# Performance work log

Hardware: AMD Instinct MI355X
Metric: run time of the kernel (lower is better)

The kernel has to match this reference:

```python
import jax, jax.numpy as jnp
import numpy as np

D = 1024
B, L = 4, 2048
H = 4  # num_heads
EPS = 1e-5


def setup_inputs() -> dict:
    key = jax.random.key(0)
    ks = jax.random.split(key, 32)
    s = 0.02
    def w(k, shp):
        return jax.random.normal(k, shp, dtype=jnp.float32) * s
    inp = {
        "features": jax.random.normal(ks[0], (B, L, D), dtype=jnp.float32),
        "action_mask": jax.random.randint(ks[1], (B, L), 0, 2, dtype=jnp.int32),
        "dial_mask": jax.random.randint(ks[2], (B, L), 0, 2, dtype=jnp.int32),
        "ent_mask": jax.random.randint(ks[3], (B, L), 0, 2, dtype=jnp.int32),
        "head_mask": jax.random.randint(ks[4], (B, L), 0, 2, dtype=jnp.int32),
        # 4 modality projections (stored as [in, out])
        "Wa": w(ks[5], (D, D)), "ba": jnp.zeros((D,), jnp.float32),
        "Wd": w(ks[6], (D, D)), "bd": jnp.zeros((D,), jnp.float32),
        "We": w(ks[7], (D, D)), "be": jnp.zeros((D,), jnp.float32),
        "Wh": w(ks[8], (D, D)), "bh": jnp.zeros((D,), jnp.float32),
        # MultiheadAttention in/out projections
        "Wq": w(ks[9], (D, D)), "bq": jnp.zeros((D,), jnp.float32),
        "Wk": w(ks[10], (D, D)), "bk": jnp.zeros((D,), jnp.float32),
        "Wv": w(ks[11], (D, D)), "bv": jnp.zeros((D,), jnp.float32),
        "Wo": w(ks[12], (D, D)), "bo": jnp.zeros((D,), jnp.float32),
        # consensus gate MLP: 4D -> 2D -> D
        "Wg1": w(ks[13], (4 * D, 2 * D)), "bg1": jnp.zeros((2 * D,), jnp.float32),
        "Wg2": w(ks[14], (2 * D, D)), "bg2": jnp.zeros((D,), jnp.float32),
        # LayerNorm
        "ln_g": jnp.ones((D,), jnp.float32), "ln_b": jnp.zeros((D,), jnp.float32),
    }
    return inp


def _forward(features, action_mask, dial_mask, ent_mask, head_mask,
             Wa, ba, Wd, bd, We, be, Wh, bh,
             Wq, bq, Wk, bk, Wv, bv, Wo, bo,
             Wg1, bg1, Wg2, bg2, ln_g, ln_b):
    b, l, d = features.shape
    hd = d // H
    masks = [action_mask, dial_mask, ent_mask, head_mask]
    proj = [(Wa, ba), (Wd, bd), (We, be), (Wh, bh)]
    # masked linear projections -> [B,L,4,D]
    mods = [
        (features @ W + bias) * m[..., None].astype(features.dtype)
        for (W, bias), m in zip(proj, masks)
    ]
    x = jnp.stack(mods, axis=2).reshape(b * l, 4, d)  # [N,4,D], N=B*L
    # tiny self-attention over the 4 modality tokens (dropout inactive / eval)
    q = (x @ Wq + bq).reshape(-1, 4, H, hd)
    k = (x @ Wk + bk).reshape(-1, 4, H, hd)
    v = (x @ Wv + bv).reshape(-1, 4, H, hd)
    scores = jnp.einsum('nqhd,nkhd->nhqk', q, k) / jnp.sqrt(jnp.float32(hd)).astype(x.dtype)
    attn = jax.nn.softmax(scores, axis=-1)
    ctx = jnp.einsum('nhqk,nkhd->nqhd', attn, v).reshape(-1, 4, d)
    attended = (ctx @ Wo + bo).reshape(b, l, 4 * d)
    # gate MLP (exact erf GELU, matching nn.GELU default)
    h = jax.nn.gelu(attended @ Wg1 + bg1, approximate=False)
    consensus = h @ Wg2 + bg2
    # residual + LayerNorm
    y = features + consensus
    mu = jnp.mean(y, axis=-1, keepdims=True)
    var = jnp.mean(jnp.square(y - mu), axis=-1, keepdims=True)
    return (y - mu) / jnp.sqrt(var + EPS) * ln_g + ln_b


def reference(features, action_mask, dial_mask, ent_mask, head_mask,
              Wa, ba, Wd, bd, We, be, Wh, bh,
              Wq, bq, Wk, bk, Wv, bv, Wo, bo,
              Wg1, bg1, Wg2, bg2, ln_g, ln_b):
    return _forward(features, action_mask, dial_mask, ent_mask, head_mask,
                    Wa, ba, Wd, bd, We, be, Wh, bh,
                    Wq, bq, Wk, bk, Wv, bv, Wo, bo,
                    Wg1, bg1, Wg2, bg2, ln_g, ln_b)
```

## Files before the change

### kernel.cpp

```cpp
#include <hip/hip_runtime.h>
#include <cstdint>
#include <cstddef>

#define DM   1024
#define NT   8192
#define HD   256
#define BM 128
#define BN 128
#define BK 64

typedef __attribute__((ext_vector_type(4))) float f32x4;
typedef __attribute__((ext_vector_type(8))) short bf16x8;

#define MF(a_, b_, c_) __builtin_amdgcn_mfma_f32_16x16x32_bf16(a_, b_, c_, 0, 0, 0)

__device__ __forceinline__ unsigned short f2bf(float f) {
    union { float f; uint32_t u; } v; v.f = f;
    return (unsigned short)((v.u + 0x7fffu + ((v.u >> 16) & 1u)) >> 16);
}
__device__ __forceinline__ float bf2f(unsigned short h) {
    union { uint32_t u; float f; } v; v.u = ((uint32_t)h) << 16;
    return v.f;
}

template <int SWZ>
__device__ __forceinline__ int2 swz_xy() {
    int wid = blockIdx.y * gridDim.x + blockIdx.x;
    const int nwg = gridDim.x * gridDim.y;
    int2 r;
    if (SWZ == 1 && (gridDim.x & 7) == 0) {
        const int sx = gridDim.x >> 3;
        const int c = wid & 7;
        const int l = wid >> 3;
        r.x = c * sx + l % sx;
        r.y = l / sx;
        return r;
    }
    if ((nwg & 7) == 0) {
        const int per = nwg >> 3;
        wid = (wid & 7) * per + (wid >> 3);
    }
    r.x = wid % gridDim.x;
    r.y = wid / gridDim.x;
    return r;
}

struct Ptr4 { const float* p[4]; };
struct Mask4 { const int* p[4]; };

__global__ void cvt_f32_to_bf16(const float* __restrict__ src,
                                unsigned short* __restrict__ dst, int n4) {
    int i = blockIdx.x * blockDim.x + threadIdx.x;
    if (i >= n4) return;
    float4 v = reinterpret_cast<const float4*>(src)[i];
    ushort4 o;
    o.x = f2bf(v.x); o.y = f2bf(v.y); o.z = f2bf(v.z); o.w = f2bf(v.w);
    reinterpret_cast<ushort4*>(dst)[i] = o;
}

__global__ void cvt5_f32_to_bf16(Ptr4 w4, const float* __restrict__ wo,
                                 unsigned short* __restrict__ wcat,
                                 unsigned short* __restrict__ wobf) {
    const int i = blockIdx.x * blockDim.x + threadIdx.x;
    const int w = i >> 18, r = i & 262143;
    const float* src = (w < 4) ? w4.p[w] : wo;
    unsigned short* dst = (w < 4) ? (wcat + ((size_t)w << 20)) : wobf;
    float4 v = reinterpret_cast<const float4*>(src)[r];
    ushort4 o;
    o.x = f2bf(v.x); o.y = f2bf(v.y); o.z = f2bf(v.z); o.w = f2bf(v.w);
    reinterpret_cast<ushort4*>(dst)[r] = o;
}

__global__ void transpose_cvt(const float* __restrict__ src,
                              unsigned short* __restrict__ dst, int K, int Nc) {
    __shared__ float tile[32][33];
    const int n0 = blockIdx.x * 32, k0 = blockIdx.y * 32;
    const int tx = threadIdx.x & 31, ty = threadIdx.x >> 5;
#pragma unroll
    for (int i = 0; i < 4; ++i) {
        int k = ty + i * 8;
        tile[k][tx] = src[(size_t)(k0 + k) * Nc + n0 + tx];
    }
    __syncthreads();
#pragma unroll
    for (int i = 0; i < 4; ++i) {
        int n = ty + i * 8;
        dst[(size_t)(n0 + n) * K + k0 + tx] = f2bf(tile[tx][n]);
    }
}

__device__ __forceinline__ void gload16(const void* g, void* l) {
    __builtin_amdgcn_global_load_lds(
        (const __attribute__((address_space(1))) void*)g,
        (__attribute__((address_space(3))) void*)l, 16, 0, 0);
}

template <int EPI, int SWZ = 0>
__global__ void gemm_bt(const unsigned short* __restrict__ A,
                        const unsigned short* __restrict__ Bt,
                        void* __restrict__ out, Ptr4 bias, Mask4 masks,
                        const float* __restrict__ biasA,
                        int M, int Nc, int K) {
    __shared__ __attribute__((aligned(16))) unsigned short Als[BM * BK];
    __shared__ __attribute__((aligned(16))) unsigned short Bls[BN * BK];
    const int tid = threadIdx.x;
    const int wave = tid >> 6, lane = tid & 63;
    const int2 bxy = swz_xy<SWZ>();
    const int tileM = bxy.y * BM, tileN = bxy.x * BN;
    const int wr = wave >> 1, wc = wave & 1;
    const int la = lane & 15, lh = lane >> 4;

    f32x4 acc[4][4] = {};

    const int sr = tid >> 3;
    const int sb = (tid & 7) * 16;
    const int ssw = (sb ^ ((sr & 7) << 4)) >> 1;
    const unsigned short* aSrcs[4];
    const unsigned short* bSrcs[4];
#pragma unroll
    for (int c = 0; c < 4; ++c) {
        aSrcs[c] = A + (size_t)(tileM + c * 32 + sr) * K + ssw;
        bSrcs[c] = Bt + (size_t)(tileN + c * 32 + sr) * K + ssw;
    }

    for (int k0 = 0; k0 < K; k0 += BK) {
#pragma unroll
        for (int c = 0; c < 4; ++c)
            gload16(aSrcs[c] + k0, &Als[wave * 512 + c * 2048]);
#pragma unroll
        for (int c = 0; c < 4; ++c)
            gload16(bSrcs[c] + k0, &Bls[wave * 512 + c * 2048]);
        __syncthreads();
#pragma unroll
        for (int ks = 0; ks < 2; ++ks) {
            const int uo = ((ks * 4 + lh) ^ (la & 7)) * 8;
            bf16x8 af[4], bfr[4];
#pragma unroll
            for (int m = 0; m < 4; ++m)
                af[m] = *reinterpret_cast<const bf16x8*>(&Als[(wr * 64 + m * 16 + la) * BK + uo]);
#pragma unroll
            for (int n = 0; n < 4; ++n)
                bfr[n] = *reinterpret_cast<const bf16x8*>(&Bls[(wc * 64 + n * 16 + la) * BK + uo]);
#pragma unroll
            for (int m = 0; m < 4; ++m)
#pragma unroll
                for (int n = 0; n < 4; ++n)
                    acc[m][n] = MF(af[m], bfr[n], acc[m][n]);
        }
        __syncthreads();
    }

    const int rowT = tileM + wr * 64 + lh * 4;
    const int colT = tileN + wc * 64;
    unsigned short* outB = (unsigned short*)out;
    float* outF = (float*)out;

    float mv[4][4];
    if constexpr (EPI == 0 || EPI == 5) {
        const int* mp = (EPI == 0) ? masks.p[tileN >> 10] : masks.p[(tileN >> 10) & 3];
#pragma unroll
        for (int m = 0; m < 4; ++m)
#pragma unroll
            for (int i = 0; i < 4; ++i)
                mv[m][i] = (float)mp[rowT + m * 16 + i];
    }
    const float* bp = nullptr;
    const float* bp2 = nullptr;
    if constexpr (EPI == 5) bp2 = bias.p[tileN >> 12];
    else bp = bias.p[tileN >> 10];

#pragma unroll
    for (int n = 0; n < 4; ++n) {
        const int gcol = colT + n * 16 + la;
        float bv, bv2 = 0.f;
        if constexpr (EPI == 5) { bv = biasA[gcol]; bv2 = bp2[gcol & (DM - 1)]; }
        else bv = bp[gcol & (DM - 1)];
#pragma unroll
        for (int m = 0; m < 4; ++m) {
#pragma unroll
            for (int i = 0; i < 4; ++i) {
                const int grow = rowT + m * 16 + i;
                float val = acc[m][n][i] + bv;
                if constexpr (EPI == 0) {
                    val *= mv[m][i];
                    outB[(size_t)grow * Nc + gcol] = f2bf(val);
                } else if constexpr (EPI == 1) {
                    outB[(size_t)grow * Nc + gcol] = f2bf(val);
                } else if constexpr (EPI == 2) {
                    val = 0.5f * val * (1.0f + erff(val * 0.70710678118654752f));
                    outB[(size_t)grow * Nc + gcol] = f2bf(val);
                } else if constexpr (EPI == 3) {
                    outF[(size_t)grow * Nc + gcol] = val;
                } else {
                    val = mv[m][i] * val + bv2;
                    outB[(size_t)grow * Nc + gcol] = f2bf(val);
                }
            }
        }
    }
}

template <bool TSTORE>
__global__ void gemm_prep(const unsigned short* __restrict__ A0, int lda, int aZoff,
                          const unsigned short* __restrict__ Bt, int ldb,
                          unsigned short* __restrict__ out, int ldc, int cZstride,
                          int K) {
    __shared__ __attribute__((aligned(16))) unsigned short Als[BM * BK];
    __shared__ __attribute__((aligned(16))) unsigned short Bls[BN * BK];
    const unsigned short* A = A0 + (size_t)blockIdx.z * aZoff;
    const int tid = threadIdx.x;
    const int wave = tid >> 6, lane = tid & 63;
    const int2 bxy = swz_xy<0>();
    const int tileM = bxy.y * BM, tileN = bxy.x * BN;
    const int wr = wave >> 1, wc = wave & 1;
    const int la = lane & 15, lh = lane >> 4;

    f32x4 acc[4][4] = {};

    const int sr = tid >> 3;
    const int sb = (tid & 7) * 16;
    const int ssw = (sb ^ ((sr & 7) << 4)) >> 1;
    const unsigned short* aSrcs[4];
    const unsigned short* bSrcs[4];
#pragma unroll
    for (int c = 0; c < 4; ++c) {
        aSrcs[c] = A + (size_t)(tileM + c * 32 + sr) * lda + ssw;
        bSrcs[c] = Bt + (size_t)(tileN + c * 32 + sr) * ldb + ssw;
    }

    for (int k0 = 0; k0 < K; k0 += BK) {
#pragma unroll
        for (int c = 0; c < 4; ++c)
            gload16(aSrcs[c] + k0, &Als[wave * 512 + c * 2048]);
#pragma unroll
        for (int c = 0; c < 4; ++c)
            gload16(bSrcs[c] + k0, &Bls[wave * 512 + c * 2048]);
        __syncthreads();
#pragma unroll
        for (int ks = 0; ks < 2; ++ks) {
            const int uo = ((ks * 4 + lh) ^ (la & 7)) * 8;
            bf16x8 af[4], bfr[4];
#pragma unroll
            for (int m = 0; m < 4; ++m)
                af[m] = *reinterpret_cast<const bf16x8*>(&Als[(wr * 64 + m * 16 + la) * BK + uo]);
#pragma unroll
            for (int n = 0; n < 4; ++n)
                bfr[n] = *reinterpret_cast<const bf16x8*>(&Bls[(wc * 64 + n * 16 + la) * BK + uo]);
#pragma unroll
            for (int m = 0; m < 4; ++m)
#pragma unroll
                for (int n = 0; n < 4; ++n)
                    acc[m][n] = MF(af[m], bfr[n], acc[m][n]);
        }
        __syncthreads();
    }

    const int rowT = tileM + wr * 64 + lh * 4;
    const int colT = tileN + wc * 64;

#pragma unroll
    for (int n = 0; n < 4; ++n) {
        const int gcol = colT + n * 16 + la;
#pragma unroll
        for (int m = 0; m < 4; ++m) {
            if constexpr (TSTORE) {
                const int g0 = rowT + m * 16;
                ushort4 o4;
                o4.x = f2bf(acc[m][n][0]);
                o4.y = f2bf(acc[m][n][1]);
                o4.z = f2bf(acc[m][n][2]);
                o4.w = f2bf(acc[m][n][3]);
                const size_t drow = ((size_t)(gcol >> 10) << 12) +
                                    ((size_t)(g0 >> 10) << 10) + (gcol & 1023);
                *reinterpret_cast<ushort4*>(out + drow * 1024 + (g0 & 1023)) = o4;
            } else {
#pragma unroll
                for (int i = 0; i < 4; ++i) {
                    const int grow = rowT + m * 16 + i;
                    out[(size_t)grow * ldc + (size_t)blockIdx.z * cZstride + gcol] =
                        f2bf(acc[m][n][i]);
                }
            }
        }
    }
}

__global__ void fuse_biasA(Ptr4 bmods, const unsigned short* __restrict__ Btqkv,
                           float* __restrict__ biasA) {
    const int o = blockIdx.x * 4 + (threadIdx.x >> 6);
    const int lane = threadIdx.x & 63;
    const int qk = o >> 12, im = (o >> 10) & 3, j = o & 1023;
    const float* b = bmods.p[im];
    const unsigned short* wrow = Btqkv + ((size_t)(qk << 10) + j) * 1024;
    float s = 0.f;
    for (int t = lane; t < 1024; t += 64) s += b[t] * bf2f(wrow[t]);
#pragma unroll
    for (int off = 32; off >= 1; off >>= 1) s += __shfl_xor(s, off, 64);
    if (lane == 0) biasA[o] = s;
}

__global__ void fuse_biasH(const float* __restrict__ bo, const float* __restrict__ bg1,
                           const unsigned short* __restrict__ Btg1,
                           float* __restrict__ biasH) {
    const int c = blockIdx.x * 4 + (threadIdx.x >> 6);
    const int lane = threadIdx.x & 63;
    const unsigned short* row = Btg1 + (size_t)c * 4096;
    float s = 0.f;
    for (int t = lane; t < 4096; t += 64) s += bo[t & 1023] * bf2f(row[t]);
#pragma unroll
    for (int off = 32; off >= 1; off >>= 1) s += __shfl_xor(s, off, 64);
    if (lane == 0) biasH[c] = s + bg1[c];
}

__global__ void attn4F(const unsigned short* __restrict__ qkvF,
                       unsigned short* __restrict__ ctx) {
    const int n = blockIdx.x;
    const int h = threadIdx.x >> 6;
    const int lane = threadIdx.x & 63;
    const size_t base = (size_t)n * 12288 + h * HD + lane * 4;

    float q[4][4], k[4][4], v[4][4];
#pragma unroll
    for (int m = 0; m < 4; ++m) {
        ushort4 uq = *reinterpret_cast<const ushort4*>(&qkvF[base + m * 1024]);
        ushort4 uk = *reinterpret_cast<const ushort4*>(&qkvF[base + m * 1024 + 4096]);
        ushort4 uv = *reinterpret_cast<const ushort4*>(&qkvF[base + m * 1024 + 8192]);
        q[m][0] = bf2f(uq.x); q[m][1] = bf2f(uq.y); q[m][2] = bf2f(uq.z); q[m][3] = bf2f(uq.w);
        k[m][0] = bf2f(uk.x); k[m][1] = bf2f(uk.y); k[m][2] = bf2f(uk.z); k[m][3] = bf2f(uk.w);
        v[m][0] = bf2f(uv.x); v[m][1] = bf2f(uv.y); v[m][2] = bf2f(uv.z); v[m][3] = bf2f(uv.w);
    }

    float s[4][4];
#pragma unroll
    for (int qi = 0; qi < 4; ++qi)
#pragma unroll
        for (int ki = 0; ki < 4; ++ki)
            s[qi][ki] = q[qi][0] * k[ki][0] + q[qi][1] * k[ki][1] +
                        q[qi][2] * k[ki][2] + q[qi][3] * k[ki][3];
#pragma unroll
    for (int off = 32; off >= 1; off >>= 1) {
#pragma unroll
        for (int qi = 0; qi < 4; ++qi)
#pragma unroll
            for (int ki = 0; ki < 4; ++ki)
                s[qi][ki] += __shfl_xor(s[qi][ki], off, 64);
    }

#pragma unroll
    for (int qi = 0; qi < 4; ++qi) {
        float s0 = s[qi][0] * 0.0625f, s1 = s[qi][1] * 0.0625f;
        float s2 = s[qi][2] * 0.0625f, s3 = s[qi][3] * 0.0625f;
        float mx = fmaxf(fmaxf(s0, s1), fmaxf(s2, s3));
        float e0 = __expf(s0 - mx), e1 = __expf(s1 - mx);
        float e2 = __expf(s2 - mx), e3 = __expf(s3 - mx);
        float inv = 1.0f / (e0 + e1 + e2 + e3);
        e0 *= inv; e1 *= inv; e2 *= inv; e3 *= inv;
        ushort4 o;
        o.x = f2bf(e0 * v[0][0] + e1 * v[1][0] + e2 * v[2][0] + e3 * v[3][0]);
        o.y = f2bf(e0 * v[0][1] + e1 * v[1][1] + e2 * v[2][1] + e3 * v[3][1]);
        o.z = f2bf(e0 * v[0][2] + e1 * v[1][2] + e2 * v[2][2] + e3 * v[3][2]);
        o.w = f2bf(e0 * v[0][3] + e1 * v[1][3] + e2 * v[2][3] + e3 * v[3][3]);
        *reinterpret_cast<ushort4*>(&ctx[(size_t)n * 4096 + qi * 1024 + h * HD + lane * 4]) = o;
    }
}

__global__ void attn4(const unsigned short* __restrict__ qkv,
                      unsigned short* __restrict__ ctx) {
    const int n = blockIdx.x;
    const int h = threadIdx.x >> 6;
    const int lane = threadIdx.x & 63;
    const size_t base = (size_t)n * 4 * 3072 + h * HD + lane * 4;

    float q[4][4], k[4][4], v[4][4];
#pragma unroll
    for (int m = 0; m < 4; ++m) {
        ushort4 uq = *reinterpret_cast<const ushort4*>(&qkv[base + (size_t)m * 3072]);
        ushort4 uk = *reinterpret_cast<const ushort4*>(&qkv[base + (size_t)m * 3072 + 1024]);
        ushort4 uv = *reinterpret_cast<const ushort4*>(&qkv[base + (size_t)m * 3072 + 2048]);
        q[m][0] = bf2f(uq.x); q[m][1] = bf2f(uq.y); q[m][2] = bf2f(uq.z); q[m][3] = bf2f(uq.w);
        k[m][0] = bf2f(uk.x); k[m][1] = bf2f(uk.y); k[m][2] = bf2f(uk.z); k[m][3] = bf2f(uk.w);
        v[m][0] = bf2f(uv.x); v[m][1] = bf2f(uv.y); v[m][2] = bf2f(uv.z); v[m][3] = bf2f(uv.w);
    }

    float s[4][4];
#pragma unroll
    for (int qi = 0; qi < 4; ++qi)
#pragma unroll
        for (int ki = 0; ki < 4; ++ki)
            s[qi][ki] = q[qi][0] * k[ki][0] + q[qi][1] * k[ki][1] +
                        q[qi][2] * k[ki][2] + q[qi][3] * k[ki][3];
#pragma unroll
    for (int off = 32; off >= 1; off >>= 1) {
#pragma unroll
        for (int qi = 0; qi < 4; ++qi)
#pragma unroll
            for (int ki = 0; ki < 4; ++ki)
                s[qi][ki] += __shfl_xor(s[qi][ki], off, 64);
    }

#pragma unroll
    for (int qi = 0; qi < 4; ++qi) {
        float s0 = s[qi][0] * 0.0625f, s1 = s[qi][1] * 0.0625f;
        float s2 = s[qi][2] * 0.0625f, s3 = s[qi][3] * 0.0625f;
        float mx = fmaxf(fmaxf(s0, s1), fmaxf(s2, s3));
        float e0 = __expf(s0 - mx), e1 = __expf(s1 - mx);
        float e2 = __expf(s2 - mx), e3 = __expf(s3 - mx);
        float inv = 1.0f / (e0 + e1 + e2 + e3);
        e0 *= inv; e1 *= inv; e2 *= inv; e3 *= inv;
        ushort4 o;
        o.x = f2bf(e0 * v[0][0] + e1 * v[1][0] + e2 * v[2][0] + e3 * v[3][0]);
        o.y = f2bf(e0 * v[0][1] + e1 * v[1][1] + e2 * v[2][1] + e3 * v[3][1]);
        o.z = f2bf(e0 * v[0][2] + e1 * v[1][2] + e2 * v[2][2] + e3 * v[3][2]);
        o.w = f2bf(e0 * v[0][3] + e1 * v[1][3] + e2 * v[2][3] + e3 * v[3][3]);
        *reinterpret_cast<ushort4*>(&ctx[(size_t)(n * 4 + qi) * 1024 + h * HD + lane * 4]) = o;
    }
}

__global__ void resid_ln(const float* __restrict__ cons, const float* __restrict__ feat,
                         const float* __restrict__ g, const float* __restrict__ b,
                         float* __restrict__ out) {
    const int row = blockIdx.x;
    const int t = threadIdx.x;
    const size_t base = (size_t)row * DM + t * 4;
    float4 c = *reinterpret_cast<const float4*>(&cons[base]);
    float4 f = *reinterpret_cast<const float4*>(&feat[base]);
    float y0 = c.x + f.x, y1 = c.y + f.y, y2 = c.z + f.z, y3 = c.w + f.w;
    float sum = y0 + y1 + y2 + y3;
    float sq = y0 * y0 + y1 * y1 + y2 * y2 + y3 * y3;
#pragma unroll
    for (int off = 32; off >= 1; off >>= 1) {
        sum += __shfl_xor(sum, off, 64);
        sq += __shfl_xor(sq, off, 64);
    }
    __shared__ float rs[4], rq[4];
    const int wv = t >> 6, ln = t & 63;
    if (ln == 0) { rs[wv] = sum; rq[wv] = sq; }
    __syncthreads();
    sum = rs[0] + rs[1] + rs[2] + rs[3];
    sq = rq[0] + rq[1] + rq[2] + rq[3];
    const float mu = sum * (1.0f / DM);
    const float var = sq * (1.0f / DM) - mu * mu;
    const float rstd = rsqrtf(var + 1e-5f);
    float4 gg = *reinterpret_cast<const float4*>(&g[t * 4]);
    float4 bb = *reinterpret_cast<const float4*>(&b[t * 4]);
    float4 o;
    o.x = (y0 - mu) * rstd * gg.x + bb.x;
    o.y = (y1 - mu) * rstd * gg.y + bb.y;
    o.z = (y2 - mu) * rstd * gg.z + bb.z;
    o.w = (y3 - mu) * rstd * gg.w + bb.w;
    *reinterpret_cast<float4*>(&out[base]) = o;
}

extern "C" void kernel_launch(void* const* d_in, const int* in_sizes, int n_in,
                              void* d_out, int out_size, void* d_ws, size_t ws_size,
                              hipStream_t stream) {
    (void)in_sizes; (void)n_in; (void)out_size;
    const float* feat = (const float*)d_in[0];
    const int* am = (const int*)d_in[1];
    const int* dmk = (const int*)d_in[2];
    const int* em = (const int*)d_in[3];
    const int* hmk = (const int*)d_in[4];
    const float* Wa = (const float*)d_in[5];  const float* ba = (const float*)d_in[6];
    const float* Wd = (const float*)d_in[7];  const float* bd = (const float*)d_in[8];
    const float* We = (const float*)d_in[9];  const float* be = (const float*)d_in[10];
    const float* Wh = (const float*)d_in[11]; const float* bh = (const float*)d_in[12];
    const float* Wq = (const float*)d_in[13]; const float* bq = (const float*)d_in[14];
    const float* Wk = (const float*)d_in[15]; const float* bk = (const float*)d_in[16];
    const float* Wv = (const float*)d_in[17]; const float* bv = (const float*)d_in[18];
    const float* Wo = (const float*)d_in[19]; const float* bo = (const float*)d_in[20];
    const float* Wg1 = (const float*)d_in[21]; const float* bg1 = (const float*)d_in[22];
    const float* Wg2 = (const float*)d_in[23]; const float* bg2 = (const float*)d_in[24];
    const float* lng = (const float*)d_in[25]; const float* lnb = (const float*)d_in[26];

    char* ws = (char*)d_ws;
    size_t off = 0;
    auto take = [&](size_t bytes) -> char* {
        char* r = ws + off;
        off = (off + bytes + 255) & ~(size_t)255;
        return r;
    };
    unsigned short* featB = (unsigned short*)take((size_t)NT * DM * 2);
    unsigned short* Btqkv = (unsigned short*)take((size_t)3 * DM * DM * 2);
    unsigned short* Btg1  = (unsigned short*)take((size_t)2 * DM * 4 * DM * 2);
    unsigned short* Btg2  = (unsigned short*)take((size_t)DM * 2 * DM * 2);
    unsigned short* Wcat  = (unsigned short*)take((size_t)4 * DM * DM * 2);
    unsigned short* Wo_bf = (unsigned short*)take((size_t)DM * DM * 2);
    unsigned short* Btf   = (unsigned short*)take((size_t)12 * DM * DM * 2);
    unsigned short* Btm1  = (unsigned short*)take((size_t)8 * DM * DM * 2);
    float* biasA          = (float*)take((size_t)12 * DM * 4);
    float* biasH          = (float*)take((size_t)2 * DM * 4);
    const size_t fixed = off;

    cvt_f32_to_bf16<<<dim3((NT * DM / 4 + 255) / 256), dim3(256), 0, stream>>>(
        feat, featB, NT * DM / 4);
    auto tl = [&](const float* src, unsigned short* dst, int K, int Nc) {
        transpose_cvt<<<dim3(Nc / 32, K / 32), dim3(256), 0, stream>>>(src, dst, K, Nc);
    };
    tl(Wq, Btqkv, DM, DM);
    tl(Wk, Btqkv + (size_t)DM * DM, DM, DM);
    tl(Wv, Btqkv + (size_t)2 * DM * DM, DM, DM);
    tl(Wg1, Btg1, 4 * DM, 2 * DM);
    tl(Wg2, Btg2, 2 * DM, DM);

    Ptr4 bmods{{ba, bd, be, bh}};
    Ptr4 bqkv{{bq, bk, bv, nullptr}};
    Ptr4 bH{{biasH, biasH + DM, nullptr, nullptr}};
    Ptr4 bg24{{bg2, nullptr, nullptr, nullptr}};
    Mask4 mnull{{nullptr, nullptr, nullptr, nullptr}};

    const size_t ctxBytes = (size_t)NT * 4096 * 2;
    const size_t hBytes = (size_t)NT * 2048 * 2 + 512;
    int T2 = 0;
    {
        const int cands[4] = {8192, 4096, 2048, 1024};
        for (int ci = 0; ci < 4; ++ci) {
            int c = cands[ci];
            size_t chunkB = (size_t)c * 24576 + 512;
            size_t regHB = chunkB > hBytes ? chunkB : hBytes;
            if (fixed + ctxBytes + 256 + regHB + 4096 <= ws_size) { T2 = c; break; }
        }
    }

    if (T2 > 0) {
        char* regX = take(ctxBytes);
        size_t chunkB = (size_t)T2 * 24576 + 512;
        char* regH = take(chunkB > hBytes ? chunkB : hBytes);
        unsigned short* ctx = (unsigned short*)regX;
        float* cons = (float*)regX;
        unsigned short* h = (unsigned short*)regH;
        unsigned short* qkvF = (unsigned short*)regH;

        Ptr4 w4{{Wa, Wd, We, Wh}};
        cvt5_f32_to_bf16<<<dim3(5 * DM * DM / 4 / 256), dim3(256), 0, stream>>>(
            w4, Wo, Wcat, Wo_bf);
        gemm_prep<true><<<dim3(24, 32, 1), dim3(256), 0, stream>>>(
            Wcat, DM, 0, Btqkv, DM, Btf, 0, 0, DM);
        gemm_prep<false><<<dim3(8, 16, 4), dim3(256), 0, stream>>>(
            Btg1, 4 * DM, DM, Wo_bf, DM, Btm1, 4 * DM, DM, DM);
        fuse_biasA<<<dim3(12 * DM / 4), dim3(256), 0, stream>>>(bmods, Btqkv, biasA);
        fuse_biasH<<<dim3(2 * DM / 4), dim3(256), 0, stream>>>(bo, bg1, Btg1, biasH);

        for (int t0 = 0; t0 < NT; t0 += T2) {
            Mask4 mk{{am + t0, dmk + t0, em + t0, hmk + t0}};
            gemm_bt<5, 1><<<dim3(96, T2 / BM), dim3(256), 0, stream>>>(
                featB + (size_t)t0 * DM, Btf, (void*)qkvF, bqkv, mk, biasA,
                T2, 12 * DM, DM);
            attn4F<<<dim3(T2), dim3(256), 0, stream>>>(qkvF, ctx + (size_t)t0 * 4096);
        }
        gemm_bt<2><<<dim3(16, NT / BM), dim3(256), 0, stream>>>(
            ctx, Btm1, (void*)h, bH, mnull, nullptr, NT, 2 * DM, 4 * DM);
        gemm_bt<3><<<dim3(8, NT / BM), dim3(256), 0, stream>>>(
            h, Btg2, (void*)cons, bg24, mnull, nullptr, NT, DM, 2 * DM);
        resid_ln<<<dim3(NT), dim3(256), 0, stream>>>(cons, feat, lng, lnb, (float*)d_out);
        return;
    }

    unsigned short* Bt1 = (unsigned short*)take((size_t)4 * DM * DM * 2);
    unsigned short* Bto = (unsigned short*)take((size_t)DM * DM * 2);
    tl(Wa, Bt1, DM, DM);
    tl(Wd, Bt1 + (size_t)DM * DM, DM, DM);
    tl(We, Bt1 + (size_t)2 * DM * DM, DM, DM);
    tl(Wh, Bt1 + (size_t)3 * DM * DM, DM, DM);
    tl(Wo, Bto, DM, DM);

    Ptr4 b1{{ba, bd, be, bh}};
    Ptr4 bo4{{bo, nullptr, nullptr, nullptr}};
    Ptr4 bg14{{bg1, bg1 + DM, nullptr, nullptr}};

    const size_t avail = (ws_size > off) ? (ws_size - off) : 0;
    int T = 2048;
    while (T > 128 && ((size_t)T * 40960 + 4096) > avail) T >>= 1;
    unsigned short* bufA = (unsigned short*)take((size_t)T * 4096 * 2);
    unsigned short* bufB = (unsigned short*)take((size_t)T * 4 * 3072 * 2);
    unsigned short* bufC = (unsigned short*)take((size_t)T * 4 * 1024 * 2);

    const int nch = NT / T;
    for (int c = 0; c < nch; ++c) {
        const int t0 = c * T;
        Mask4 mk{{am + t0, dmk + t0, em + t0, hmk + t0}};
        gemm_bt<0><<<dim3(4 * DM / BN, T / BM), dim3(256), 0, stream>>>(
            featB + (size_t)t0 * DM, Bt1, (void*)bufA, b1, mk, nullptr, T, 4 * DM, DM);
        gemm_bt<1><<<dim3(3 * DM / BN, 4 * T / BM), dim3(256), 0, stream>>>(
            bufA, Btqkv, (void*)bufB, bqkv, mnull, nullptr, 4 * T, 3 * DM, DM);
        attn4<<<dim3(T), dim3(256), 0, stream>>>(bufB, bufC);
        gemm_bt<1><<<dim3(DM / BN, 4 * T / BM), dim3(256), 0, stream>>>(
            bufC, Bto, (void*)bufA, bo4, mnull, nullptr, 4 * T, DM, DM);
        gemm_bt<2><<<dim3(2 * DM / BN, T / BM), dim3(256), 0, stream>>>(
            bufA, Btg1, (void*)bufC, bg14, mnull, nullptr, T, 2 * DM, 4 * DM);
        gemm_bt<3><<<dim3(DM / BN, T / BM), dim3(256), 0, stream>>>(
            bufC, Btg2, (void*)bufB, bg24, mnull, nullptr, T, DM, 2 * DM);
        resid_ln<<<dim3(T), dim3(256), 0, stream>>>(
            (const float*)bufB, feat + (size_t)t0 * DM, lng, lnb,
            (float*)d_out + (size_t)t0 * DM);
    }
}
```

Baseline: 588.5 us.

## Switch GEMMs to 32x32x16 MFMA with fragment-major LDS layout; bf16 consensus output

Both GEMM kernels move from 16x16x32 MFMA with a 4x4 accumulator grid to 32x32x16 MFMA with a 2x2 grid of 16-wide accumulators. Global-to-LDS loads are rearranged so each 32-row by 8-column fragment is stored contiguously, letting each lane read its operand with one linear LDS access and no XOR swizzle. The aim is fewer MFMA and LDS instructions per K step. Separately, the consensus GEMM now writes bf16 instead of fp32 and the residual LayerNorm reads bf16, halving that buffer's traffic at the cost of some precision before the normalization.

Measured after the change: 988.1 us. +67.9%, slower.

```diff
diff --git a/kernel.cpp b/kernel.cpp
--- a/kernel.cpp
+++ b/kernel.cpp
@@ -10,9 +10,10 @@
 #define BK 64
 
 typedef __attribute__((ext_vector_type(4))) float f32x4;
+typedef __attribute__((ext_vector_type(16))) float f32x16;
 typedef __attribute__((ext_vector_type(8))) short bf16x8;
 
-#define MF(a_, b_, c_) __builtin_amdgcn_mfma_f32_16x16x32_bf16(a_, b_, c_, 0, 0, 0)
+#define MF32(a_, b_, c_) __builtin_amdgcn_mfma_f32_32x32x16_bf16(a_, b_, c_, 0, 0, 0)
 
 __device__ __forceinline__ unsigned short f2bf(float f) {
     union { float f; uint32_t u; } v; v.f = f;
@@ -108,92 +109,84 @@
     const int2 bxy = swz_xy<SWZ>();
     const int tileM = bxy.y * BM, tileN = bxy.x * BN;
     const int wr = wave >> 1, wc = wave & 1;
-    const int la = lane & 15, lh = lane >> 4;
-
-    f32x4 acc[4][4] = {};
-
-    const int sr = tid >> 3;
-    const int sb = (tid & 7) * 16;
-    const int ssw = (sb ^ ((sr & 7) << 4)) >> 1;
+    const int la32 = lane & 31, lh32 = lane >> 5;
+
+    f32x16 acc[2][2] = {};
+
     const unsigned short* aSrcs[4];
     const unsigned short* bSrcs[4];
 #pragma unroll
-    for (int c = 0; c < 4; ++c) {
-        aSrcs[c] = A + (size_t)(tileM + c * 32 + sr) * K + ssw;
-        bSrcs[c] = Bt + (size_t)(tileN + c * 32 + sr) * K + ssw;
+    for (int r = 0; r < 4; ++r) {
+        aSrcs[r] = A + (size_t)(tileM + r * 32 + la32) * K + wave * 16 + lh32 * 8;
+        bSrcs[r] = Bt + (size_t)(tileN + r * 32 + la32) * K + wave * 16 + lh32 * 8;
     }
 
     for (int k0 = 0; k0 < K; k0 += BK) {
 #pragma unroll
-        for (int c = 0; c < 4; ++c)
-            gload16(aSrcs[c] + k0, &Als[wave * 512 + c * 2048]);
-#pragma unroll
-        for (int c = 0; c < 4; ++c)
-            gload16(bSrcs[c] + k0, &Bls[wave * 512 + c * 2048]);
+        for (int r = 0; r < 4; ++r)
+            gload16(aSrcs[r] + k0, &Als[r * 2048 + wave * 512]);
+#pragma unroll
+        for (int r = 0; r < 4; ++r)
+            gload16(bSrcs[r] + k0, &Bls[r * 2048 + wave * 512]);
         __syncthreads();
 #pragma unroll
-        for (int ks = 0; ks < 2; ++ks) {
-            const int uo = ((ks * 4 + lh) ^ (la & 7)) * 8;
-            bf16x8 af[4], bfr[4];
-#pragma unroll
-            for (int m = 0; m < 4; ++m)
-                af[m] = *reinterpret_cast<const bf16x8*>(&Als[(wr * 64 + m * 16 + la) * BK + uo]);
-#pragma unroll
-            for (int n = 0; n < 4; ++n)
-                bfr[n] = *reinterpret_cast<const bf16x8*>(&Bls[(wc * 64 + n * 16 + la) * BK + uo]);
-#pragma unroll
-            for (int m = 0; m < 4; ++m)
-#pragma unroll
-                for (int n = 0; n < 4; ++n)
-                    acc[m][n] = MF(af[m], bfr[n], acc[m][n]);
+        for (int ks = 0; ks < 4; ++ks) {
+            bf16x8 af[2], bfr[2];
+#pragma unroll
+            for (int mt = 0; mt < 2; ++mt)
+                af[mt] = *reinterpret_cast<const bf16x8*>(
+                    &Als[((wr * 2 + mt) * 4 + ks) * 512 + lane * 8]);
+#pragma unroll
+            for (int nt = 0; nt < 2; ++nt)
+                bfr[nt] = *reinterpret_cast<const bf16x8*>(
+                    &Bls[((wc * 2 + nt) * 4 + ks) * 512 + lane * 8]);
+#pragma unroll
+            for (int mt = 0; mt < 2; ++mt)
+#pragma unroll
+                for (int nt = 0; nt < 2; ++nt)
+                    acc[mt][nt] = MF32(af[mt], bfr[nt], acc[mt][nt]);
         }
         __syncthreads();
     }
 
-    const int rowT = tileM + wr * 64 + lh * 4;
-    const int colT = tileN + wc * 64;
     unsigned short* outB = (unsigned short*)out;
-    float* outF = (float*)out;
-
-    float mv[4][4];
-    if constexpr (EPI == 0 || EPI == 5) {
-        const int* mp = (EPI == 0) ? masks.p[tileN >> 10] : masks.p[(tileN >> 10) & 3];
-#pragma unroll
-        for (int m = 0; m < 4; ++m)
-#pragma unroll
-            for (int i = 0; i < 4; ++i)
-                mv[m][i] = (float)mp[rowT + m * 16 + i];
-    }
+    const int* mp = nullptr;
+    if constexpr (EPI == 0) mp = masks.p[tileN >> 10];
+    if constexpr (EPI == 5) mp = masks.p[(tileN >> 10) & 3];
     const float* bp = nullptr;
     const float* bp2 = nullptr;
     if constexpr (EPI == 5) bp2 = bias.p[tileN >> 12];
     else bp = bias.p[tileN >> 10];
 
 #pragma unroll
-    for (int n = 0; n < 4; ++n) {
-        const int gcol = colT + n * 16 + la;
+    for (int nt = 0; nt < 2; ++nt) {
+        const int gcol = tileN + (wc * 2 + nt) * 32 + la32;
         float bv, bv2 = 0.f;
         if constexpr (EPI == 5) { bv = biasA[gcol]; bv2 = bp2[gcol & (DM - 1)]; }
         else bv = bp[gcol & (DM - 1)];
 #pragma unroll
-        for (int m = 0; m < 4; ++m) {
-#pragma unroll
-            for (int i = 0; i < 4; ++i) {
-                const int grow = rowT + m * 16 + i;
-                float val = acc[m][n][i] + bv;
-                if constexpr (EPI == 0) {
-                    val *= mv[m][i];
-                    outB[(size_t)grow * Nc + gcol] = f2bf(val);
-                } else if constexpr (EPI == 1) {
-                    outB[(size_t)grow * Nc + gcol] = f2bf(val);
-                } else if constexpr (EPI == 2) {
-                    val = 0.5f * val * (1.0f + erff(val * 0.70710678118654752f));
-                    outB[(size_t)grow * Nc + gcol] = f2bf(val);
-                } else if constexpr (EPI == 3) {
-                    outF[(size_t)grow * Nc + gcol] = val;
-                } else {
-                    val = mv[m][i] * val + bv2;
-                    outB[(size_t)grow * Nc + gcol] = f2bf(val);
+        for (int mt = 0; mt < 2; ++mt) {
+#pragma unroll
+            for (int rg = 0; rg < 4; ++rg) {
+                const int rowb = tileM + (wr * 2 + mt) * 32 + lh32 * 4 + rg * 8;
+#pragma unroll
+                for (int i = 0; i < 4; ++i) {
+                    const int grow = rowb + i;
+                    float val = acc[mt][nt][rg * 4 + i] + bv;
+                    if constexpr (EPI == 0) {
+                        val *= (float)mp[grow];
+                        outB[(size_t)grow * Nc + gcol] = f2bf(val);
+                    } else if constexpr (EPI == 1) {
+                        outB[(size_t)grow * Nc + gcol] = f2bf(val);
+                    } else if constexpr (EPI == 2) {
+                        val = 0.5f * val * (1.0f + erff(val * 0.70710678118654752f));
+                        outB[(size_t)grow * Nc + gcol] = f2bf(val);
+                    } else if constexpr (EPI == 3) {
+                        outB[(size_t)grow * Nc + gcol] = f2bf(val);
+                    } else {
+                        val = (float)mp[grow] * val + bv2;
+                        outB[(size_t)grow * Nc + gcol] = f2bf(val);
+                    }
                 }
             }
         }
@@ -213,72 +206,70 @@
     const int2 bxy = swz_xy<0>();
     const int tileM = bxy.y * BM, tileN = bxy.x * BN;
     const int wr = wave >> 1, wc = wave & 1;
-    const int la = lane & 15, lh = lane >> 4;
-
-    f32x4 acc[4][4] = {};
-
-    const int sr = tid >> 3;
-    const int sb = (tid & 7) * 16;
-    const int ssw = (sb ^ ((sr & 7) << 4)) >> 1;
+    const int la32 = lane & 31, lh32 = lane >> 5;
+
+    f32x16 acc[2][2] = {};
+
     const unsigned short* aSrcs[4];
     const unsigned short* bSrcs[4];
 #pragma unroll
-    for (int c = 0; c < 4; ++c) {
-        aSrcs[c] = A + (size_t)(tileM + c * 32 + sr) * lda + ssw;
-        bSrcs[c] = Bt + (size_t)(tileN + c * 32 + sr) * ldb + ssw;
+    for (int r = 0; r < 4; ++r) {
+        aSrcs[r] = A + (size_t)(tileM + r * 32 + la32) * lda + wave * 16 + lh32 * 8;
+        bSrcs[r] = Bt + (size_t)(tileN + r * 32 + la32) * ldb + wave * 16 + lh32 * 8;
     }
 
     for (int k0 = 0; k0 < K; k0 += BK) {
 #pragma unroll
-        for (int c = 0; c < 4; ++c)
-            gload16(aSrcs[c] + k0, &Als[wave * 512 + c * 2048]);
-#pragma unroll
-        for (int c = 0; c < 4; ++c)
-            gload16(bSrcs[c] + k0, &Bls[wave * 512 + c * 2048]);
+        for (int r = 0; r < 4; ++r)
+            gload16(aSrcs[r] + k0, &Als[r * 2048 + wave * 512]);
+#pragma unroll
+        for (int r = 0; r < 4; ++r)
+            gload16(bSrcs[r] + k0, &Bls[r * 2048 + wave * 512]);
         __syncthreads();
 #pragma unroll
-        for (int ks = 0; ks < 2; ++ks) {
-            const int uo = ((ks * 4 + lh) ^ (la & 7)) * 8;
-            bf16x8 af[4], bfr[4];
-#pragma unroll
-            for (int m = 0; m < 4; ++m)
-                af[m] = *reinterpret_cast<const bf16x8*>(&Als[(wr * 64 + m * 16 + la) * BK + uo]);
-#pragma unroll
-            for (int n = 0; n < 4; ++n)
-                bfr[n] = *reinterpret_cast<const bf16x8*>(&Bls[(wc * 64 + n * 16 + la) * BK + uo]);
-#pragma unroll
-            for (int m = 0; m < 4; ++m)
-#pragma unroll
-                for (int n = 0; n < 4; ++n)
-                    acc[m][n] = MF(af[m], bfr[n], acc[m][n]);
+        for (int ks = 0; ks < 4; ++ks) {
+            bf16x8 af[2], bfr[2];
+#pragma unroll
+            for (int mt = 0; mt < 2; ++mt)
+                af[mt] = *reinterpret_cast<const bf16x8*>(
+                    &Als[((wr * 2 + mt) * 4 + ks) * 512 + lane * 8]);
+#pragma unroll
+            for (int nt = 0; nt < 2; ++nt)
+                bfr[nt] = *reinterpret_cast<const bf16x8*>(
+                    &Bls[((wc * 2 + nt) * 4 + ks) * 512 + lane * 8]);
+#pragma unroll
+            for (int mt = 0; mt < 2; ++mt)
+#pragma unroll
+                for (int nt = 0; nt < 2; ++nt)
+                    acc[mt][nt] = MF32(af[mt], bfr[nt], acc[mt][nt]);
         }
         __syncthreads();
     }
 
-    const int rowT = tileM + wr * 64 + lh * 4;
-    const int colT = tileN + wc * 64;
-
-#pragma unroll
-    for (int n = 0; n < 4; ++n) {
-        const int gcol = colT + n * 16 + la;
-#pragma unroll
-        for (int m = 0; m < 4; ++m) {
-            if constexpr (TSTORE) {
-                const int g0 = rowT + m * 16;
-                ushort4 o4;
-                o4.x = f2bf(acc[m][n][0]);
-                o4.y = f2bf(acc[m][n][1]);
-                o4.z = f2bf(acc[m][n][2]);
-                o4.w = f2bf(acc[m][n][3]);
-                const size_t drow = ((size_t)(gcol >> 10) << 12) +
-                                    ((size_t)(g0 >> 10) << 10) + (gcol & 1023);
-                *reinterpret_cast<ushort4*>(out + drow * 1024 + (g0 & 1023)) = o4;
-            } else {
-#pragma unroll
-                for (int i = 0; i < 4; ++i) {
-                    const int grow = rowT + m * 16 + i;
-                    out[(size_t)grow * ldc + (size_t)blockIdx.z * cZstride + gcol] =
-                        f2bf(acc[m][n][i]);
+#pragma unroll
+    for (int nt = 0; nt < 2; ++nt) {
+        const int gcol = tileN + (wc * 2 + nt) * 32 + la32;
+#pragma unroll
+        for (int mt = 0; mt < 2; ++mt) {
+#pragma unroll
+            for (int rg = 0; rg < 4; ++rg) {
+                const int g0 = tileM + (wr * 2 + mt) * 32 + lh32 * 4 + rg * 8;
+                if constexpr (TSTORE) {
+                    ushort4 o4;
+                    o4.x = f2bf(acc[mt][nt][rg * 4 + 0]);
+                    o4.y = f2bf(acc[mt][nt][rg * 4 + 1]);
+                    o4.z = f2bf(acc[mt][nt][rg * 4 + 2]);
+                    o4.w = f2bf(acc[mt][nt][rg * 4 + 3]);
+                    const size_t drow = ((size_t)(gcol >> 10) << 12) +
+                                        ((size_t)(g0 >> 10) << 10) + (gcol & 1023);
+                    *reinterpret_cast<ushort4*>(out + drow * 1024 + (g0 & 1023)) = o4;
+                } else {
+#pragma unroll
+                    for (int i = 0; i < 4; ++i) {
+                        const int grow = g0 + i;
+                        out[(size_t)grow * ldc + (size_t)blockIdx.z * cZstride + gcol] =
+                            f2bf(acc[mt][nt][rg * 4 + i]);
+                    }
                 }
             }
         }
@@ -416,15 +407,17 @@
     }
 }
 
-__global__ void resid_ln(const float* __restrict__ cons, const float* __restrict__ feat,
+__global__ void resid_ln(const unsigned short* __restrict__ cons,
+                         const float* __restrict__ feat,
                          const float* __restrict__ g, const float* __restrict__ b,
                          float* __restrict__ out) {
     const int row = blockIdx.x;
     const int t = threadIdx.x;
     const size_t base = (size_t)row * DM + t * 4;
-    float4 c = *reinterpret_cast<const float4*>(&cons[base]);
+    ushort4 c4 = *reinterpret_cast<const ushort4*>(&cons[base]);
     float4 f = *reinterpret_cast<const float4*>(&feat[base]);
-    float y0 = c.x + f.x, y1 = c.y + f.y, y2 = c.z + f.z, y3 = c.w + f.w;
+    float y0 = bf2f(c4.x) + f.x, y1 = bf2f(c4.y) + f.y;
+    float y2 = bf2f(c4.z) + f.z, y3 = bf2f(c4.w) + f.w;
     float sum = y0 + y1 + y2 + y3;
     float sq = y0 * y0 + y1 * y1 + y2 * y2 + y3 * y3;
 #pragma unroll
@@ -526,7 +519,7 @@
         size_t chunkB = (size_t)T2 * 24576 + 512;
         char* regH = take(chunkB > hBytes ? chunkB : hBytes);
         unsigned short* ctx = (unsigned short*)regX;
-        float* cons = (float*)regX;
+        unsigned short* cons = (unsigned short*)regX;
         unsigned short* h = (unsigned short*)regH;
         unsigned short* qkvF = (unsigned short*)regH;
 
@@ -590,7 +583,7 @@
         gemm_bt<3><<<dim3(DM / BN, T / BM), dim3(256), 0, stream>>>(
             bufC, Btg2, (void*)bufB, bg24, mnull, nullptr, T, DM, 2 * DM);
         resid_ln<<<dim3(T), dim3(256), 0, stream>>>(
-            (const float*)bufB, feat + (size_t)t0 * DM, lng, lnb,
+            bufB, feat + (size_t)t0 * DM, lng, lnb,
             (float*)d_out + (size_t)t0 * DM);
     }
 }
```

## Add two-wave 128x128 GEMM variant and store consensus in bf16

Applied to the files above, without the earlier changes.

Adds gemm_bt2, which computes a 128x128 tile with 2 waves of 128 threads instead of 4. Each wave holds an 8x4 grid of MFMA accumulators, which raises register reuse of A fragments and is declared with launch bounds allowing 2 blocks per CU. It is used for the fused QKV projection GEMM and the gate GEMM1. Separately, the consensus GEMM output is now written as bf16 instead of fp32 and read as bf16 in the residual LayerNorm, halving that intermediate's traffic at some precision cost. The larger accumulator tile raises register pressure and may lower occupancy.

New measurement: 741.8 us. +26.1%, slower.

```diff
diff --git a/kernel.cpp b/kernel.cpp
--- a/kernel.cpp
+++ b/kernel.cpp
@@ -153,7 +153,6 @@
     const int rowT = tileM + wr * 64 + lh * 4;
     const int colT = tileN + wc * 64;
     unsigned short* outB = (unsigned short*)out;
-    float* outF = (float*)out;
 
     float mv[4][4];
     if constexpr (EPI == 0 || EPI == 5) {
@@ -190,9 +189,102 @@
                     val = 0.5f * val * (1.0f + erff(val * 0.70710678118654752f));
                     outB[(size_t)grow * Nc + gcol] = f2bf(val);
                 } else if constexpr (EPI == 3) {
-                    outF[(size_t)grow * Nc + gcol] = val;
+                    outB[(size_t)grow * Nc + gcol] = f2bf(val);
                 } else {
                     val = mv[m][i] * val + bv2;
+                    outB[(size_t)grow * Nc + gcol] = f2bf(val);
+                }
+            }
+        }
+    }
+}
+
+template <int EPI, int SWZ = 0>
+__global__ __launch_bounds__(128, 2)
+void gemm_bt2(const unsigned short* __restrict__ A,
+              const unsigned short* __restrict__ Bt,
+              void* __restrict__ out, Ptr4 bias, Mask4 masks,
+              const float* __restrict__ biasA,
+              int M, int Nc, int K) {
+    __shared__ __attribute__((aligned(16))) unsigned short Als[BM * BK];
+    __shared__ __attribute__((aligned(16))) unsigned short Bls[BN * BK];
+    const int tid = threadIdx.x;
+    const int wave = tid >> 6, lane = tid & 63;
+    const int2 bxy = swz_xy<SWZ>();
+    const int tileM = bxy.y * BM, tileN = bxy.x * BN;
+    const int la = lane & 15, lh = lane >> 4;
+
+    f32x4 acc[8][4] = {};
+
+    const int sr = tid >> 3;
+    const int sb = (tid & 7) * 16;
+    const int ssw = (sb ^ ((sr & 7) << 4)) >> 1;
+    const unsigned short* aBase = A + (size_t)(tileM + sr) * K + ssw;
+    const unsigned short* bBase = Bt + (size_t)(tileN + sr) * K + ssw;
+
+    for (int k0 = 0; k0 < K; k0 += BK) {
+#pragma unroll
+        for (int c = 0; c < 8; ++c)
+            gload16(aBase + (size_t)(c * 16) * K + k0, &Als[c * 1024 + wave * 512]);
+#pragma unroll
+        for (int c = 0; c < 8; ++c)
+            gload16(bBase + (size_t)(c * 16) * K + k0, &Bls[c * 1024 + wave * 512]);
+        __syncthreads();
+#pragma unroll
+        for (int ks = 0; ks < 2; ++ks) {
+            const int uo = ((ks * 4 + lh) ^ (la & 7)) * 8;
+            bf16x8 af[8], bfr[4];
+#pragma unroll
+            for (int m = 0; m < 8; ++m)
+                af[m] = *reinterpret_cast<const bf16x8*>(&Als[(m * 16 + la) * BK + uo]);
+#pragma unroll
+            for (int n = 0; n < 4; ++n)
+                bfr[n] = *reinterpret_cast<const bf16x8*>(&Bls[(wave * 64 + n * 16 + la) * BK + uo]);
+#pragma unroll
+            for (int m = 0; m < 8; ++m)
+#pragma unroll
+                for (int n = 0; n < 4; ++n)
+                    acc[m][n] = MF(af[m], bfr[n], acc[m][n]);
+        }
+        __syncthreads();
+    }
+
+    const int rowT = tileM + lh * 4;
+    const int colT = tileN + wave * 64;
+    unsigned short* outB = (unsigned short*)out;
+
+    const int* mp = nullptr;
+    if constexpr (EPI == 0) mp = masks.p[tileN >> 10];
+    if constexpr (EPI == 5) mp = masks.p[(tileN >> 10) & 3];
+    const float* bp = nullptr;
+    const float* bp2 = nullptr;
+    if constexpr (EPI == 5) bp2 = bias.p[tileN >> 12];
+    else bp = bias.p[tileN >> 10];
+
+#pragma unroll
+    for (int n = 0; n < 4; ++n) {
+        const int gcol = colT + n * 16 + la;
+        float bv, bv2 = 0.f;
+        if constexpr (EPI == 5) { bv = biasA[gcol]; bv2 = bp2[gcol & (DM - 1)]; }
+        else bv = bp[gcol & (DM - 1)];
+#pragma unroll
+        for (int m = 0; m < 8; ++m) {
+#pragma unroll
+            for (int i = 0; i < 4; ++i) {
+                const int grow = rowT + m * 16 + i;
+                float val = acc[m][n][i] + bv;
+                if constexpr (EPI == 0) {
+                    val *= (float)mp[grow];
+                    outB[(size_t)grow * Nc + gcol] = f2bf(val);
+                } else if constexpr (EPI == 1) {
+                    outB[(size_t)grow * Nc + gcol] = f2bf(val);
+                } else if constexpr (EPI == 2) {
+                    val = 0.5f * val * (1.0f + erff(val * 0.70710678118654752f));
+                    outB[(size_t)grow * Nc + gcol] = f2bf(val);
+                } else if constexpr (EPI == 3) {
+                    outB[(size_t)grow * Nc + gcol] = f2bf(val);
+                } else {
+                    val = (float)mp[grow] * val + bv2;
                     outB[(size_t)grow * Nc + gcol] = f2bf(val);
                 }
             }
@@ -416,15 +508,17 @@
     }
 }
 
-__global__ void resid_ln(const float* __restrict__ cons, const float* __restrict__ feat,
+__global__ void resid_ln(const unsigned short* __restrict__ cons,
+                         const float* __restrict__ feat,
                          const float* __restrict__ g, const float* __restrict__ b,
                          float* __restrict__ out) {
     const int row = blockIdx.x;
     const int t = threadIdx.x;
     const size_t base = (size_t)row * DM + t * 4;
-    float4 c = *reinterpret_cast<const float4*>(&cons[base]);
+    ushort4 c4 = *reinterpret_cast<const ushort4*>(&cons[base]);
     float4 f = *reinterpret_cast<const float4*>(&feat[base]);
-    float y0 = c.x + f.x, y1 = c.y + f.y, y2 = c.z + f.z, y3 = c.w + f.w;
+    float y0 = bf2f(c4.x) + f.x, y1 = bf2f(c4.y) + f.y;
+    float y2 = bf2f(c4.z) + f.z, y3 = bf2f(c4.w) + f.w;
     float sum = y0 + y1 + y2 + y3;
     float sq = y0 * y0 + y1 * y1 + y2 * y2 + y3 * y3;
 #pragma unroll
@@ -526,7 +620,7 @@
         size_t chunkB = (size_t)T2 * 24576 + 512;
         char* regH = take(chunkB > hBytes ? chunkB : hBytes);
         unsigned short* ctx = (unsigned short*)regX;
-        float* cons = (float*)regX;
+        unsigned short* cons = (unsigned short*)regX;
         unsigned short* h = (unsigned short*)regH;
         unsigned short* qkvF = (unsigned short*)regH;
 
@@ -542,12 +636,12 @@
 
         for (int t0 = 0; t0 < NT; t0 += T2) {
             Mask4 mk{{am + t0, dmk + t0, em + t0, hmk + t0}};
-            gemm_bt<5, 1><<<dim3(96, T2 / BM), dim3(256), 0, stream>>>(
+            gemm_bt2<5, 1><<<dim3(96, T2 / BM), dim3(128), 0, stream>>>(
                 featB + (size_t)t0 * DM, Btf, (void*)qkvF, bqkv, mk, biasA,
                 T2, 12 * DM, DM);
             attn4F<<<dim3(T2), dim3(256), 0, stream>>>(qkvF, ctx + (size_t)t0 * 4096);
         }
-        gemm_bt<2><<<dim3(16, NT / BM), dim3(256), 0, stream>>>(
+        gemm_bt2<2, 0><<<dim3(16, NT / BM), dim3(128), 0, stream>>>(
             ctx, Btm1, (void*)h, bH, mnull, nullptr, NT, 2 * DM, 4 * DM);
         gemm_bt<3><<<dim3(8, NT / BM), dim3(256), 0, stream>>>(
             h, Btg2, (void*)cons, bg24, mnull, nullptr, NT, DM, 2 * DM);
@@ -590,7 +684,7 @@
         gemm_bt<3><<<dim3(DM / BN, T / BM), dim3(256), 0, stream>>>(
             bufC, Btg2, (void*)bufB, bg24, mnull, nullptr, T, DM, 2 * DM);
         resid_ln<<<dim3(T), dim3(256), 0, stream>>>(
-            (const float*)bufB, feat + (size_t)t0 * DM, lng, lnb,
+            bufB, feat + (size_t)t0 * DM, lng, lnb,
             (float*)d_out + (size_t)t0 * DM);
     }
 }
```
